# Kernel optimization log

Hardware: AMD Instinct MI355X
Metric: run time of the kernel (lower is better)

## Reference

```python
import jax, jax.numpy as jnp
import numpy as np

N, C, H, W = 64, 128, 32, 32
EPS = 1e-5


def _layernorm_chw(x, w, b):
    # LayerNorm over normalized_shape=(C,H,W): last 3 dims
    mu = jnp.mean(x, axis=(1, 2, 3), keepdims=True)
    var = jnp.var(x, axis=(1, 2, 3), keepdims=True)
    return (x - mu) * jax.lax.rsqrt(var + EPS) * w[None] + b[None]


def _conv1x1(x, w, b):
    # x: [N,C,H,W], w: [Cout,Cin], b: [Cout]
    return jnp.einsum('oc,nchw->nohw', w, x) + b[None, :, None, None]


def setup_inputs() -> dict:
    key = jax.random.key(0)
    ks = jax.random.split(key, 12)
    d = {
        'query': jax.random.normal(ks[0], (N, C, H, W), jnp.float32),
        'key': jax.random.normal(ks[1], (N, C, H, W), jnp.float32),
        'value': jax.random.normal(ks[2], (N, C, H, W), jnp.float32),
        'ln1_w': jnp.ones((C, H, W), jnp.float32),
        'ln1_b': jnp.zeros((C, H, W), jnp.float32),
        'ln2_w': jnp.ones((C, H, W), jnp.float32),
        'ln2_b': jnp.zeros((C, H, W), jnp.float32),
        'ln3_w': jnp.ones((C, H, W), jnp.float32),
        'ln3_b': jnp.zeros((C, H, W), jnp.float32),
        'wq': jax.random.normal(ks[3], (C, C), jnp.float32) / np.sqrt(C),
        'bq': jnp.zeros((C,), jnp.float32),
        'wk': jax.random.normal(ks[4], (C, C), jnp.float32) / np.sqrt(C),
        'bk': jnp.zeros((C,), jnp.float32),
        'wv': jax.random.normal(ks[5], (C, C), jnp.float32) / np.sqrt(C),
        'bv': jnp.zeros((C,), jnp.float32),
    }
    return d


def reference(query, key, value, ln1_w, ln1_b, ln2_w, ln2_b, ln3_w, ln3_b,
              wq, bq, wk, bk, wv, bv):
    qn = _layernorm_chw(query, ln1_w, ln1_b)  # residual uses normalized query
    kn = _layernorm_chw(key, ln2_w, ln2_b)
    vn = _layernorm_chw(value, ln3_w, ln3_b)
    q = _conv1x1(qn, wq, bq).reshape(N, C, H * W)
    k = _conv1x1(kn, wk, bk).reshape(N, C, H * W)
    v = _conv1x1(vn, wv, bv).reshape(N, C, H * W)
    # attention[n,i,j] = sum_c k[n,c,i] q[n,c,j] / sqrt(C); softmax over i (dim=1)
    attn = jnp.einsum('nci,ncj->nij', k, q) / jnp.sqrt(jnp.float32(C))
    attn = jax.nn.softmax(attn, axis=1)
    out = jnp.einsum('nci,nij->ncj', v, attn).reshape(N, C, H, W)
    x = qn + out
    return x.reshape(N, -1)  # flatten(start_dim=1)
```

## Files before the change

### kernel.cpp

```cpp
#include <hip/hip_runtime.h>


#define NS 64
#define CD 128
#define SD 1024
#define MEL (CD*SD)
#define SCALE 0.08838834764831845f

typedef __attribute__((ext_vector_type(4))) float floatx4;
typedef __attribute__((ext_vector_type(8))) short short8;
typedef __attribute__((ext_vector_type(4))) short short4v;

typedef __attribute__((address_space(1))) const void global_cvoid;
typedef __attribute__((address_space(3))) void lds_void;

__device__ __forceinline__ void gl16(const void* g, void* l) {
  __builtin_amdgcn_global_load_lds((global_cvoid*)g, (lds_void*)l, 16, 0, 0);
}
__device__ __forceinline__ unsigned short f2bf(float f) {
  union { float f; unsigned int i; } v; v.f = f;
  unsigned int i = v.i;
  return (unsigned short)((i + 0x7fffu + ((i >> 16) & 1u)) >> 16);
}
__device__ __forceinline__ short8 ld8_bf16(const float* __restrict__ p) {
  floatx4 a = *(const floatx4*)p;
  floatx4 b = *(const floatx4*)(p + 4);
  short8 r;
  r[0] = (short)f2bf(a[0]); r[1] = (short)f2bf(a[1]);
  r[2] = (short)f2bf(a[2]); r[3] = (short)f2bf(a[3]);
  r[4] = (short)f2bf(b[0]); r[5] = (short)f2bf(b[1]);
  r[6] = (short)f2bf(b[2]); r[7] = (short)f2bf(b[3]);
  return r;
}
__device__ __forceinline__ floatx4 mfma16(short8 a, short8 b, floatx4 c) {
  return __builtin_amdgcn_mfma_f32_16x16x32_bf16(a, b, c, 0, 0, 0);
}

__global__ __launch_bounds__(512) void stats_kernel(
    const float* __restrict__ q, const float* __restrict__ k,
    const float* __restrict__ v, float* __restrict__ sums)
{
  int tn = blockIdx.x;
  int t = tn >> 6;
  const float* x = (t == 0 ? q : (t == 1 ? k : v)) + (size_t)(tn & 63) * MEL;
  float s1 = 0.f, s2 = 0.f;
  for (int it = 0; it < 64; ++it) {
    floatx4 u = *(const floatx4*)(x + it * 2048 + threadIdx.x * 4);
#pragma unroll
    for (int j = 0; j < 4; ++j) { float f = u[j]; s1 += f; s2 += f * f; }
  }
#pragma unroll
  for (int off = 32; off; off >>= 1) {
    s1 += __shfl_xor(s1, off, 64);
    s2 += __shfl_xor(s2, off, 64);
  }
  __shared__ float r1[8], r2[8];
  int w = threadIdx.x >> 6;
  if ((threadIdx.x & 63) == 0) { r1[w] = s1; r2[w] = s2; }
  __syncthreads();
  if (threadIdx.x == 0) {
    float a = 0.f, b = 0.f;
#pragma unroll
    for (int i = 0; i < 8; ++i) { a += r1[i]; b += r2[i]; }
    sums[tn] = a; sums[192 + tn] = b;
  }
}

__global__ __launch_bounds__(512, 4) void proj_kernel(
  const float* __restrict__ k, const float* __restrict__ v,
  const float* __restrict__ l2w, const float* __restrict__ l2b,
  const float* __restrict__ l3w, const float* __restrict__ l3b,
  const float* __restrict__ wk, const float* __restrict__ bk,
  const float* __restrict__ wv, const float* __restrict__ bv,
  const float* __restrict__ sums,
  unsigned short* __restrict__ kT, unsigned short* __restrict__ vN)
{
  int n  = blockIdx.x, t = blockIdx.y, st = blockIdx.z;
  const float* x  = (t == 0 ? k : v) + (size_t)n * MEL;
  const float* lw = (t == 0 ? l2w : l3w);
  const float* lb = (t == 0 ? l2b : l3b);
  const float* W  = (t == 0 ? wk : wv);
  const float* Bs = (t == 0 ? bk : bv);

  float mu  = sums[(t + 1) * 64 + n] * (1.f / MEL);
  float var = sums[192 + (t + 1) * 64 + n] * (1.f / MEL) - mu * mu;
  float rs  = rsqrtf(var + 1e-5f);
  float a_ln = rs, b_ln = -mu * rs;

  __shared__ __align__(16) unsigned short Xt[128 * 136];

  int tid = threadIdx.x;
  int cb = tid & 15, sb = (tid >> 4) & 15, half = tid >> 8;
  int s0 = st * 128;

  unsigned int w32[8][2];
#pragma unroll
  for (int pr = 0; pr < 2; ++pr) {
    int c0 = cb * 8 + half * 4 + pr * 2;
    const float* xp0 = x  + (size_t)c0 * SD + s0 + sb * 8;
    const float* wp0 = lw + (size_t)c0 * SD + s0 + sb * 8;
    const float* bp0 = lb + (size_t)c0 * SD + s0 + sb * 8;
    float xv0[8], xv1[8], wv0[8], wv1[8], bv0[8], bv1[8];
    *(floatx4*)xv0 = *(const floatx4*)xp0;       *(floatx4*)(xv0+4) = *(const floatx4*)(xp0+4);
    *(floatx4*)xv1 = *(const floatx4*)(xp0+SD);  *(floatx4*)(xv1+4) = *(const floatx4*)(xp0+SD+4);
    *(floatx4*)wv0 = *(const floatx4*)wp0;       *(floatx4*)(wv0+4) = *(const floatx4*)(wp0+4);
    *(floatx4*)wv1 = *(const floatx4*)(wp0+SD);  *(floatx4*)(wv1+4) = *(const floatx4*)(wp0+SD+4);
    *(floatx4*)bv0 = *(const floatx4*)bp0;       *(floatx4*)(bv0+4) = *(const floatx4*)(bp0+4);
    *(floatx4*)bv1 = *(const floatx4*)(bp0+SD);  *(floatx4*)(bv1+4) = *(const floatx4*)(bp0+SD+4);
#pragma unroll
    for (int js = 0; js < 8; ++js) {
      unsigned int lo = f2bf((xv0[js] * a_ln + b_ln) * wv0[js] + bv0[js]);
      unsigned int hi = f2bf((xv1[js] * a_ln + b_ln) * wv1[js] + bv1[js]);
      w32[js][pr] = lo | (hi << 16);
    }
  }
#pragma unroll
  for (int js = 0; js < 8; ++js) {
    unsigned int* d = (unsigned int*)&Xt[(sb * 8 + js) * 136 + cb * 8 + half * 4];
    d[0] = w32[js][0]; d[1] = w32[js][1];
  }
  __syncthreads();

  int lane = tid & 63, w = tid >> 6;
  int quad = lane >> 4, l16 = lane & 15;

  short8 Af[4];
#pragma unroll
  for (int kk = 0; kk < 4; ++kk)
    Af[kk] = ld8_bf16(W + (w * 16 + l16) * CD + kk * 32 + quad * 8);

  floatx4 acc[8];
  floatx4 zz = {0.f, 0.f, 0.f, 0.f};
#pragma unroll
  for (int nb = 0; nb < 8; ++nb) acc[nb] = zz;
#pragma unroll
  for (int kk = 0; kk < 4; ++kk)
#pragma unroll
    for (int nb = 0; nb < 8; ++nb) {
      short8 Bf = *(const short8*)&Xt[(nb * 16 + l16) * 136 + kk * 32 + quad * 8];
      acc[nb] = mfma16(Af[kk], Bf, acc[nb]);
    }

  float bsv[4];
#pragma unroll
  for (int r = 0; r < 4; ++r) bsv[r] = Bs[w * 16 + quad * 4 + r];

  if (t == 0) {
#pragma unroll
    for (int nb = 0; nb < 8; ++nb) {
      short4v pk;
#pragma unroll
      for (int r = 0; r < 4; ++r) pk[r] = (short)f2bf(acc[nb][r] + bsv[r]);
      size_t g = (size_t)n * MEL + (size_t)(s0 + nb * 16 + l16) * CD + w * 16 + quad * 4;
      *(short4v*)(kT + g) = pk;
    }
  } else {
#pragma unroll
    for (int nb = 0; nb < 8; ++nb)
#pragma unroll
      for (int r = 0; r < 4; ++r) {
        size_t g = (size_t)n * MEL + (size_t)(w * 16 + quad * 4 + r) * SD + s0 + nb * 16 + l16;
        vN[g] = f2bf(acc[nb][r] + bsv[r]);
      }
  }
}

__global__ __launch_bounds__(256, 2) void attn_kernel(
  const float* __restrict__ qraw, const float* __restrict__ l1w,
  const float* __restrict__ l1b, const float* __restrict__ wq,
  const float* __restrict__ bq,
  const unsigned short* __restrict__ kT, const unsigned short* __restrict__ vN,
  const float* __restrict__ sums, float* __restrict__ out)
{
  int n = blockIdx.x, jt = blockIdx.y;
  int j0 = jt * 128;

  __shared__ __align__(16) char smem[51712];
  unsigned short* Xt = (unsigned short*)smem;
  unsigned short* Ks = (unsigned short*)smem;
  unsigned short* Vs = (unsigned short*)(smem + 16384);
  unsigned short* Ps = (unsigned short*)(smem + 34816);
  float* l_s = (float*)(smem + 51200);

  int tid = threadIdx.x, lane = tid & 63, w = tid >> 6;
  int quad = lane >> 4, l16 = lane & 15;

  float mu  = sums[n] * (1.f / MEL);
  float var = sums[192 + n] * (1.f / MEL) - mu * mu;
  float rsd = rsqrtf(var + 1e-5f);
  float a_ln = rsd, b_ln = -mu * rsd;
  const float* qb = qraw + (size_t)n * MEL;

  {
    int cb = tid & 15, sb = tid >> 4;
    unsigned int w32[8][4];
#pragma unroll
    for (int pr = 0; pr < 4; ++pr) {
      int c0 = cb * 8 + pr * 2;
      const float* xp0 = qb  + (size_t)c0 * SD + j0 + sb * 8;
      const float* wp0 = l1w + (size_t)c0 * SD + j0 + sb * 8;
      const float* bp0 = l1b + (size_t)c0 * SD + j0 + sb * 8;
      float xv0[8], xv1[8], wv0[8], wv1[8], bv0[8], bv1[8];
      *(floatx4*)xv0 = *(const floatx4*)xp0;       *(floatx4*)(xv0+4) = *(const floatx4*)(xp0+4);
      *(floatx4*)xv1 = *(const floatx4*)(xp0+SD);  *(floatx4*)(xv1+4) = *(const floatx4*)(xp0+SD+4);
      *(floatx4*)wv0 = *(const floatx4*)wp0;       *(floatx4*)(wv0+4) = *(const floatx4*)(wp0+4);
      *(floatx4*)wv1 = *(const floatx4*)(wp0+SD);  *(floatx4*)(wv1+4) = *(const floatx4*)(wp0+SD+4);
      *(floatx4*)bv0 = *(const floatx4*)bp0;       *(floatx4*)(bv0+4) = *(const floatx4*)(bp0+4);
      *(floatx4*)bv1 = *(const floatx4*)(bp0+SD);  *(floatx4*)(bv1+4) = *(const floatx4*)(bp0+SD+4);
#pragma unroll
      for (int js = 0; js < 8; ++js) {
        unsigned int lo = f2bf((xv0[js] * a_ln + b_ln) * wv0[js] + bv0[js]);
        unsigned int hi = f2bf((xv1[js] * a_ln + b_ln) * wv1[js] + bv1[js]);
        w32[js][pr] = lo | (hi << 16);
      }
    }
#pragma unroll
    for (int js = 0; js < 8; ++js)
      *(floatx4*)&Xt[(sb * 8 + js) * 136 + cb * 8] = *(floatx4*)w32[js];
  }
  __syncthreads();

  floatx4 zz = {0.f, 0.f, 0.f, 0.f};
  {
    short8 Af[2][4];
#pragma unroll
    for (int mi = 0; mi < 2; ++mi)
#pragma unroll
      for (int kk = 0; kk < 4; ++kk)
        Af[mi][kk] = ld8_bf16(wq + ((w * 2 + mi) * 16 + l16) * CD + kk * 32 + quad * 8);
    floatx4 accq[2][8];
#pragma unroll
    for (int mi = 0; mi < 2; ++mi)
#pragma unroll
      for (int nb = 0; nb < 8; ++nb) accq[mi][nb] = zz;
#pragma unroll
    for (int kk = 0; kk < 4; ++kk)
#pragma unroll
      for (int nb = 0; nb < 8; ++nb) {
        short8 Bf = *(const short8*)&Xt[(nb * 16 + l16) * 136 + kk * 32 + quad * 8];
        accq[0][nb] = mfma16(Af[0][kk], Bf, accq[0][nb]);
        accq[1][nb] = mfma16(Af[1][kk], Bf, accq[1][nb]);
      }
    __syncthreads();
    float bqs[2][4];
#pragma unroll
    for (int mi = 0; mi < 2; ++mi)
#pragma unroll
      for (int r = 0; r < 4; ++r) bqs[mi][r] = bq[(w * 2 + mi) * 16 + quad * 4 + r];
#pragma unroll
    for (int mi = 0; mi < 2; ++mi)
#pragma unroll
      for (int nb = 0; nb < 8; ++nb) {
        short4v pk;
#pragma unroll
        for (int r = 0; r < 4; ++r) pk[r] = (short)f2bf(accq[mi][nb][r] + bqs[mi][r]);
        *(short4v*)&Xt[(nb * 16 + l16) * 136 + (w * 2 + mi) * 16 + quad * 4] = pk;
      }
  }
  __syncthreads();

  short8 Qf[2][4];
#pragma unroll
  for (int nt = 0; nt < 2; ++nt)
#pragma unroll
    for (int kk = 0; kk < 4; ++kk)
      Qf[nt][kk] = *(const short8*)&Xt[((w * 2 + nt) * 16 + l16) * 136 + kk * 32 + quad * 8];
  __syncthreads();

  floatx4 Oc[2][8];
#pragma unroll
  for (int mi = 0; mi < 2; ++mi)
#pragma unroll
    for (int nb = 0; nb < 8; ++nb) Oc[mi][nb] = zz;
  float lsum[2] = {0.f, 0.f};

  const unsigned short* kbase0 = kT + (size_t)n * MEL;
  const unsigned short* vbase0 = vN + (size_t)n * MEL;

  for (int itile = 0; itile < 16; ++itile) {
    int i0 = itile * 64;
    const unsigned short* kbase = kbase0 + (size_t)i0 * CD;
#pragma unroll
    for (int it = 0; it < 4; ++it) {
      int nch = w * 256 + it * 64 + lane;
      int i = nch >> 4, cc = nch & 15;
      int csrc = (cc & 8) | ((cc & 7) ^ (i & 7));
      gl16(kbase + i * CD + csrc * 8, (char*)Ks + (w * 256 + it * 64) * 16);
    }
#pragma unroll
    for (int it = 0; it < 4; ++it) {
      int nch = w * 256 + it * 64 + lane;
      int c = nch >> 3, ci = nch & 7;
      int isrc = ci ^ (c & 7);
      gl16(vbase0 + (size_t)c * SD + i0 + isrc * 8, (char*)Vs + (w * 256 + it * 64) * 16);
    }
    __syncthreads();

    floatx4 Sa[4][2];
#pragma unroll
    for (int mt = 0; mt < 4; ++mt) { Sa[mt][0] = zz; Sa[mt][1] = zz; }
#pragma unroll
    for (int kk = 0; kk < 4; ++kk)
#pragma unroll
      for (int mt = 0; mt < 4; ++mt) {
        short8 Kf = *(const short8*)&Ks[(mt * 16 + l16) * 128 + (((kk * 4 + quad) ^ (l16 & 7)) * 8)];
        Sa[mt][0] = mfma16(Kf, Qf[0][kk], Sa[mt][0]);
        Sa[mt][1] = mfma16(Kf, Qf[1][kk], Sa[mt][1]);
      }

#pragma unroll
    for (int nt = 0; nt < 2; ++nt) {
      int jrow = (w * 2 + nt) * 16 + l16;
      int rowbase = jrow * 64;
      int sub = (quad & 1) * 4;
#pragma unroll
      for (int mt = 0; mt < 4; ++mt) {
        float p0 = __expf(Sa[mt][nt][0] * SCALE);
        float p1 = __expf(Sa[mt][nt][1] * SCALE);
        float p2 = __expf(Sa[mt][nt][2] * SCALE);
        float p3 = __expf(Sa[mt][nt][3] * SCALE);
        lsum[nt] += (p0 + p1) + (p2 + p3);
        short4v pk;
        pk[0] = (short)f2bf(p0); pk[1] = (short)f2bf(p1);
        pk[2] = (short)f2bf(p2); pk[3] = (short)f2bf(p3);
        int ci = mt * 2 + (quad >> 1);
        int cis = ci ^ (l16 & 7);
        *(short4v*)&Ps[rowbase + cis * 8 + sub] = pk;
      }
    }
    __syncthreads();

#pragma unroll
    for (int kk = 0; kk < 2; ++kk) {
      short8 Vf[2];
#pragma unroll
      for (int mi = 0; mi < 2; ++mi) {
        int c = (w * 2 + mi) * 16 + l16;
        Vf[mi] = *(const short8*)&Vs[c * 64 + (((kk * 4 + quad) ^ (l16 & 7)) * 8)];
      }
#pragma unroll
      for (int nb = 0; nb < 8; ++nb) {
        short8 Pf = *(const short8*)&Ps[(nb * 16 + l16) * 64 + (((kk * 4 + quad) ^ (l16 & 7)) * 8)];
        Oc[0][nb] = mfma16(Vf[0], Pf, Oc[0][nb]);
        Oc[1][nb] = mfma16(Vf[1], Pf, Oc[1][nb]);
      }
    }
    __syncthreads();
  }

#pragma unroll
  for (int nt = 0; nt < 2; ++nt) {
    lsum[nt] += __shfl_xor(lsum[nt], 16, 64);
    lsum[nt] += __shfl_xor(lsum[nt], 32, 64);
  }
  if (lane < 16) { l_s[(w * 2) * 16 + l16] = lsum[0]; l_s[(w * 2 + 1) * 16 + l16] = lsum[1]; }
  __syncthreads();

  float linv[8];
#pragma unroll
  for (int nb = 0; nb < 8; ++nb) linv[nb] = 1.f / l_s[nb * 16 + l16];
#pragma unroll
  for (int mi = 0; mi < 2; ++mi) {
#pragma unroll
    for (int r = 0; r < 4; ++r) {
      int c = (w * 2 + mi) * 16 + quad * 4 + r;
      const float* qp = qb  + (size_t)c * SD + j0;
      const float* wp = l1w + (size_t)c * SD + j0;
      const float* bp = l1b + (size_t)c * SD + j0;
      float* op = out + (size_t)n * MEL + (size_t)c * SD + j0;
#pragma unroll
      for (int nb = 0; nb < 8; ++nb) {
        int j = nb * 16 + l16;
        float qn = (qp[j] * a_ln + b_ln) * wp[j] + bp[j];
        op[j] = Oc[mi][nb][r] * linv[nb] + qn;
      }
    }
  }
}

extern "C" void kernel_launch(void* const* d_in, const int* in_sizes, int n_in,
                              void* d_out, int out_size, void* d_ws, size_t ws_size,
                              hipStream_t stream)
{
  const float* q   = (const float*)d_in[0];
  const float* k   = (const float*)d_in[1];
  const float* v   = (const float*)d_in[2];
  const float* l1w = (const float*)d_in[3];
  const float* l1b = (const float*)d_in[4];
  const float* l2w = (const float*)d_in[5];
  const float* l2b = (const float*)d_in[6];
  const float* l3w = (const float*)d_in[7];
  const float* l3b = (const float*)d_in[8];
  const float* wq  = (const float*)d_in[9];
  const float* bq  = (const float*)d_in[10];
  const float* wk  = (const float*)d_in[11];
  const float* bk  = (const float*)d_in[12];
  const float* wv  = (const float*)d_in[13];
  const float* bv  = (const float*)d_in[14];

  char* ws = (char*)d_ws;
  float* sums = (float*)ws;
  unsigned short* kT = (unsigned short*)(ws + 4096);
  unsigned short* vN = kT + (size_t)NS * MEL;

  stats_kernel<<<192, 512, 0, stream>>>(q, k, v, sums);
  proj_kernel<<<dim3(64, 2, 8), 512, 0, stream>>>(k, v, l2w, l2b, l3w, l3b,
      wk, bk, wv, bv, sums, kT, vN);
  attn_kernel<<<dim3(64, 8), 256, 0, stream>>>(q, l1w, l1b, wq, bq, kT, vN,
      sums, (float*)d_out);
}
```

Before: 254.4 us.

## Double-buffer K/V tiles, keep softmax probabilities in registers, split stats reduction

The attention loop now prefetches the next K/V tile into a second LDS buffer while the current one is consumed, dropping one barrier per tile. The P matrix is no longer staged through LDS; it is packed to bf16 with a hardware convert and redistributed across lanes with shuffles. The output layout is reassigned so each wave owns whole j columns, which removes the cross-wave row-sum exchange through LDS. The stats kernel is split into eight times as many smaller blocks that combine partial sums with atomics after a memset, raising parallelism at the cost of an extra launch and nondeterministic summation order.

```diff
diff --git a/kernel.cpp b/kernel.cpp
--- a/kernel.cpp
+++ b/kernel.cpp
@@ -21,6 +21,11 @@
   union { float f; unsigned int i; } v; v.f = f;
   unsigned int i = v.i;
   return (unsigned short)((i + 0x7fffu + ((i >> 16) & 1u)) >> 16);
+}
+__device__ __forceinline__ unsigned int pkbf(float lo, float hi) {
+  unsigned int r;
+  asm("v_cvt_pk_bf16_f32 %0, %1, %2" : "=v"(r) : "v"(lo), "v"(hi));
+  return r;
 }
 __device__ __forceinline__ short8 ld8_bf16(const float* __restrict__ p) {
   floatx4 a = *(const floatx4*)p;
@@ -36,16 +41,19 @@
   return __builtin_amdgcn_mfma_f32_16x16x32_bf16(a, b, c, 0, 0, 0);
 }
 
-__global__ __launch_bounds__(512) void stats_kernel(
+__global__ __launch_bounds__(256) void stats_kernel(
     const float* __restrict__ q, const float* __restrict__ k,
     const float* __restrict__ v, float* __restrict__ sums)
 {
-  int tn = blockIdx.x;
+  int b = blockIdx.x;
+  int tn = b >> 3, part = b & 7;
   int t = tn >> 6;
-  const float* x = (t == 0 ? q : (t == 1 ? k : v)) + (size_t)(tn & 63) * MEL;
+  const float* x = (t == 0 ? q : (t == 1 ? k : v))
+                 + (size_t)(tn & 63) * MEL + part * (MEL / 8);
   float s1 = 0.f, s2 = 0.f;
-  for (int it = 0; it < 64; ++it) {
-    floatx4 u = *(const floatx4*)(x + it * 2048 + threadIdx.x * 4);
+#pragma unroll
+  for (int it = 0; it < 16; ++it) {
+    floatx4 u = *(const floatx4*)(x + it * 1024 + threadIdx.x * 4);
 #pragma unroll
     for (int j = 0; j < 4; ++j) { float f = u[j]; s1 += f; s2 += f * f; }
   }
@@ -54,15 +62,9 @@
     s1 += __shfl_xor(s1, off, 64);
     s2 += __shfl_xor(s2, off, 64);
   }
-  __shared__ float r1[8], r2[8];
-  int w = threadIdx.x >> 6;
-  if ((threadIdx.x & 63) == 0) { r1[w] = s1; r2[w] = s2; }
-  __syncthreads();
-  if (threadIdx.x == 0) {
-    float a = 0.f, b = 0.f;
-#pragma unroll
-    for (int i = 0; i < 8; ++i) { a += r1[i]; b += r2[i]; }
-    sums[tn] = a; sums[192 + tn] = b;
+  if ((threadIdx.x & 63) == 0) {
+    atomicAdd(&sums[tn], s1);
+    atomicAdd(&sums[192 + tn], s2);
   }
 }
 
@@ -165,6 +167,30 @@
   }
 }
 
+__device__ __forceinline__ void stage_tile(
+    const unsigned short* __restrict__ kbase0,
+    const unsigned short* __restrict__ vbase0,
+    char* smem, int ti, int buf, int w, int lane)
+{
+  const unsigned short* kb = kbase0 + (size_t)ti * 64 * CD;
+  char* KD = smem + buf * 16384;
+  char* VD = smem + 32768 + buf * 16384;
+#pragma unroll
+  for (int it = 0; it < 4; ++it) {
+    int nch = w * 256 + it * 64 + lane;
+    int i = nch >> 4, cc = nch & 15;
+    int csrc = (cc & 8) | ((cc & 7) ^ (i & 7));
+    gl16(kb + i * CD + csrc * 8, KD + (w * 256 + it * 64) * 16);
+  }
+#pragma unroll
+  for (int it = 0; it < 4; ++it) {
+    int nch = w * 256 + it * 64 + lane;
+    int c = nch >> 3, ci = nch & 7;
+    int isrc = ci ^ (c & 7);
+    gl16(vbase0 + (size_t)c * SD + ti * 64 + isrc * 8, VD + (w * 256 + it * 64) * 16);
+  }
+}
+
 __global__ __launch_bounds__(256, 2) void attn_kernel(
   const float* __restrict__ qraw, const float* __restrict__ l1w,
   const float* __restrict__ l1b, const float* __restrict__ wq,
@@ -175,12 +201,8 @@
   int n = blockIdx.x, jt = blockIdx.y;
   int j0 = jt * 128;
 
-  __shared__ __align__(16) char smem[51712];
+  __shared__ __align__(16) char smem[65536];
   unsigned short* Xt = (unsigned short*)smem;
-  unsigned short* Ks = (unsigned short*)smem;
-  unsigned short* Vs = (unsigned short*)(smem + 16384);
-  unsigned short* Ps = (unsigned short*)(smem + 34816);
-  float* l_s = (float*)(smem + 51200);
 
   int tid = threadIdx.x, lane = tid & 63, w = tid >> 6;
   int quad = lane >> 4, l16 = lane & 15;
@@ -267,38 +289,32 @@
       Qf[nt][kk] = *(const short8*)&Xt[((w * 2 + nt) * 16 + l16) * 136 + kk * 32 + quad * 8];
   __syncthreads();
 
-  floatx4 Oc[2][8];
-#pragma unroll
-  for (int mi = 0; mi < 2; ++mi)
-#pragma unroll
-    for (int nb = 0; nb < 8; ++nb) Oc[mi][nb] = zz;
+  floatx4 Oc[8][2];
+#pragma unroll
+  for (int mt = 0; mt < 8; ++mt) { Oc[mt][0] = zz; Oc[mt][1] = zz; }
   float lsum[2] = {0.f, 0.f};
 
   const unsigned short* kbase0 = kT + (size_t)n * MEL;
   const unsigned short* vbase0 = vN + (size_t)n * MEL;
 
+  int idx0 = l16 + ((quad & 1) << 5);
+  int idx1 = idx0 + 16;
+  bool hiq = quad >= 2;
+
+  stage_tile(kbase0, vbase0, smem, 0, 0, w, lane);
+
   for (int itile = 0; itile < 16; ++itile) {
-    int i0 = itile * 64;
-    const unsigned short* kbase = kbase0 + (size_t)i0 * CD;
-#pragma unroll
-    for (int it = 0; it < 4; ++it) {
-      int nch = w * 256 + it * 64 + lane;
-      int i = nch >> 4, cc = nch & 15;
-      int csrc = (cc & 8) | ((cc & 7) ^ (i & 7));
-      gl16(kbase + i * CD + csrc * 8, (char*)Ks + (w * 256 + it * 64) * 16);
-    }
-#pragma unroll
-    for (int it = 0; it < 4; ++it) {
-      int nch = w * 256 + it * 64 + lane;
-      int c = nch >> 3, ci = nch & 7;
-      int isrc = ci ^ (c & 7);
-      gl16(vbase0 + (size_t)c * SD + i0 + isrc * 8, (char*)Vs + (w * 256 + it * 64) * 16);
-    }
+    int buf = itile & 1;
     __syncthreads();
+    if (itile < 15) stage_tile(kbase0, vbase0, smem, itile + 1, buf ^ 1, w, lane);
+
+    const unsigned short* Ks = (const unsigned short*)(smem + buf * 16384);
+    const unsigned short* Vs = (const unsigned short*)(smem + 32768 + buf * 16384);
 
     floatx4 Sa[4][2];
 #pragma unroll
     for (int mt = 0; mt < 4; ++mt) { Sa[mt][0] = zz; Sa[mt][1] = zz; }
+    __builtin_amdgcn_s_setprio(1);
 #pragma unroll
     for (int kk = 0; kk < 4; ++kk)
 #pragma unroll
@@ -307,12 +323,11 @@
         Sa[mt][0] = mfma16(Kf, Qf[0][kk], Sa[mt][0]);
         Sa[mt][1] = mfma16(Kf, Qf[1][kk], Sa[mt][1]);
       }
-
-#pragma unroll
-    for (int nt = 0; nt < 2; ++nt) {
-      int jrow = (w * 2 + nt) * 16 + l16;
-      int rowbase = jrow * 64;
-      int sub = (quad & 1) * 4;
+    __builtin_amdgcn_s_setprio(0);
+
+    unsigned int pp[2][4][2];
+#pragma unroll
+    for (int nt = 0; nt < 2; ++nt)
 #pragma unroll
       for (int mt = 0; mt < 4; ++mt) {
         float p0 = __expf(Sa[mt][nt][0] * SCALE);
@@ -320,32 +335,39 @@
         float p2 = __expf(Sa[mt][nt][2] * SCALE);
         float p3 = __expf(Sa[mt][nt][3] * SCALE);
         lsum[nt] += (p0 + p1) + (p2 + p3);
-        short4v pk;
-        pk[0] = (short)f2bf(p0); pk[1] = (short)f2bf(p1);
-        pk[2] = (short)f2bf(p2); pk[3] = (short)f2bf(p3);
-        int ci = mt * 2 + (quad >> 1);
-        int cis = ci ^ (l16 & 7);
-        *(short4v*)&Ps[rowbase + cis * 8 + sub] = pk;
-      }
-    }
-    __syncthreads();
+        pp[nt][mt][0] = pkbf(p0, p1);
+        pp[nt][mt][1] = pkbf(p2, p3);
+      }
 
 #pragma unroll
     for (int kk = 0; kk < 2; ++kk) {
-      short8 Vf[2];
-#pragma unroll
-      for (int mi = 0; mi < 2; ++mi) {
-        int c = (w * 2 + mi) * 16 + l16;
-        Vf[mi] = *(const short8*)&Vs[c * 64 + (((kk * 4 + quad) ^ (l16 & 7)) * 8)];
-      }
-#pragma unroll
-      for (int nb = 0; nb < 8; ++nb) {
-        short8 Pf = *(const short8*)&Ps[(nb * 16 + l16) * 64 + (((kk * 4 + quad) ^ (l16 & 7)) * 8)];
-        Oc[0][nb] = mfma16(Vf[0], Pf, Oc[0][nb]);
-        Oc[1][nb] = mfma16(Vf[1], Pf, Oc[1][nb]);
-      }
-    }
-    __syncthreads();
+      short8 Pf[2];
+#pragma unroll
+      for (int nt = 0; nt < 2; ++nt) {
+        unsigned int d0a = (unsigned int)__shfl((int)pp[nt][2*kk  ][0], idx0, 64);
+        unsigned int d0b = (unsigned int)__shfl((int)pp[nt][2*kk+1][0], idx0, 64);
+        unsigned int d1a = (unsigned int)__shfl((int)pp[nt][2*kk  ][1], idx0, 64);
+        unsigned int d1b = (unsigned int)__shfl((int)pp[nt][2*kk+1][1], idx0, 64);
+        unsigned int d2a = (unsigned int)__shfl((int)pp[nt][2*kk  ][0], idx1, 64);
+        unsigned int d2b = (unsigned int)__shfl((int)pp[nt][2*kk+1][0], idx1, 64);
+        unsigned int d3a = (unsigned int)__shfl((int)pp[nt][2*kk  ][1], idx1, 64);
+        unsigned int d3b = (unsigned int)__shfl((int)pp[nt][2*kk+1][1], idx1, 64);
+        union { unsigned int u[4]; short8 s; } pu;
+        pu.u[0] = hiq ? d0b : d0a;
+        pu.u[1] = hiq ? d1b : d1a;
+        pu.u[2] = hiq ? d2b : d2a;
+        pu.u[3] = hiq ? d3b : d3a;
+        Pf[nt] = pu.s;
+      }
+      __builtin_amdgcn_s_setprio(1);
+#pragma unroll
+      for (int mt = 0; mt < 8; ++mt) {
+        short8 Vf = *(const short8*)&Vs[(mt * 16 + l16) * 64 + (((kk * 4 + quad) ^ (l16 & 7)) * 8)];
+        Oc[mt][0] = mfma16(Vf, Pf[0], Oc[mt][0]);
+        Oc[mt][1] = mfma16(Vf, Pf[1], Oc[mt][1]);
+      }
+      __builtin_amdgcn_s_setprio(0);
+    }
   }
 
 #pragma unroll
@@ -353,27 +375,22 @@
     lsum[nt] += __shfl_xor(lsum[nt], 16, 64);
     lsum[nt] += __shfl_xor(lsum[nt], 32, 64);
   }
-  if (lane < 16) { l_s[(w * 2) * 16 + l16] = lsum[0]; l_s[(w * 2 + 1) * 16 + l16] = lsum[1]; }
-  __syncthreads();
-
-  float linv[8];
-#pragma unroll
-  for (int nb = 0; nb < 8; ++nb) linv[nb] = 1.f / l_s[nb * 16 + l16];
-#pragma unroll
-  for (int mi = 0; mi < 2; ++mi) {
+  float linv0 = 1.f / lsum[0], linv1 = 1.f / lsum[1];
+  int jA = (w * 2) * 16 + l16, jB = jA + 16;
+
+#pragma unroll
+  for (int mt = 0; mt < 8; ++mt) {
 #pragma unroll
     for (int r = 0; r < 4; ++r) {
-      int c = (w * 2 + mi) * 16 + quad * 4 + r;
+      int c = mt * 16 + quad * 4 + r;
       const float* qp = qb  + (size_t)c * SD + j0;
       const float* wp = l1w + (size_t)c * SD + j0;
       const float* bp = l1b + (size_t)c * SD + j0;
       float* op = out + (size_t)n * MEL + (size_t)c * SD + j0;
-#pragma unroll
-      for (int nb = 0; nb < 8; ++nb) {
-        int j = nb * 16 + l16;
-        float qn = (qp[j] * a_ln + b_ln) * wp[j] + bp[j];
-        op[j] = Oc[mi][nb][r] * linv[nb] + qn;
-      }
+      float qnA = (qp[jA] * a_ln + b_ln) * wp[jA] + bp[jA];
+      float qnB = (qp[jB] * a_ln + b_ln) * wp[jB] + bp[jB];
+      op[jA] = Oc[mt][0][r] * linv0 + qnA;
+      op[jB] = Oc[mt][1][r] * linv1 + qnB;
     }
   }
 }
@@ -403,7 +420,8 @@
   unsigned short* kT = (unsigned short*)(ws + 4096);
   unsigned short* vN = kT + (size_t)NS * MEL;
 
-  stats_kernel<<<192, 512, 0, stream>>>(q, k, v, sums);
+  hipMemsetAsync(sums, 0, 384 * sizeof(float), stream);
+  stats_kernel<<<1536, 256, 0, stream>>>(q, k, v, sums);
   proj_kernel<<<dim3(64, 2, 8), 512, 0, stream>>>(k, v, l2w, l2b, l3w, l3b,
       wk, bk, wv, bv, sums, kT, vN);
   attn_kernel<<<dim3(64, 8), 256, 0, stream>>>(q, l1w, l1b, wq, bq, kT, vN,
```

After: 268.5 us. 1.06x slower.
